# Kernel optimization log

Hardware: AMD Instinct MI355X
Metric: run time of the kernel (lower is better)

Reference implementation:

```python
import jax, jax.numpy as jnp
import numpy as np
from jax import lax
from jax.scipy.special import logsumexp

B, S, H, T, V = 64, 512, 768, 16, 30522


def setup_inputs() -> dict:
    key = jax.random.key(0)
    ks = jax.random.split(key, 8)
    src = jax.random.randint(ks[0], (B, S), 0, V, dtype=jnp.int32)
    label = jax.random.randint(ks[1], (B, S), 0, T, dtype=jnp.int32)
    padding_mask = jnp.ones((B, S), jnp.int32)
    emb_table = jax.random.normal(ks[2], (V, H), jnp.float32) * 0.02
    W = jax.random.normal(ks[3], (H, T), jnp.float32) * 0.02
    b = jnp.zeros((T,), jnp.float32)
    start_trans = jax.random.normal(ks[4], (T,), jnp.float32) * 0.1
    end_trans = jax.random.normal(ks[5], (T,), jnp.float32) * 0.1
    transitions = jax.random.normal(ks[6], (T, T), jnp.float32) * 0.1
    return dict(src=src, label=label, padding_mask=padding_mask,
                emb_table=emb_table, W=W, b=b, start_trans=start_trans,
                end_trans=end_trans, transitions=transitions)


def crf_log_likelihood(emissions, tags, mask, start_trans, end_trans, transitions):
    # emissions [S,B,T], tags [S,B] int, mask [S,B] float. torchcrf reduction='sum'.
    nS, nB, nT = emissions.shape
    barange = jnp.arange(nB)
    # --- numerator: score of the gold path ---
    score0 = start_trans[tags[0]] + emissions[0, barange, tags[0]]
    def num_step(score, xs):
        em_t, tag_prev, tag_t, m = xs
        s = transitions[tag_prev, tag_t] + em_t[barange, tag_t]
        return score + s * m, None
    num, _ = lax.scan(num_step, score0, (emissions[1:], tags[:-1], tags[1:], mask[1:]))
    seq_len = jnp.sum(mask, axis=0).astype(jnp.int32)          # [B]
    last_tags = tags[seq_len - 1, barange]
    num = num + end_trans[last_tags]
    # --- denominator: forward algorithm (per-step logsumexp) ---
    alpha0 = start_trans[None, :] + emissions[0]               # [B,T]
    def den_step(alpha, xs):
        em_t, m = xs
        nxt = logsumexp(alpha[:, :, None] + transitions[None, :, :] + em_t[:, None, :], axis=1)
        return jnp.where(m[:, None] > 0, nxt, alpha), None
    alpha, _ = lax.scan(den_step, alpha0, (emissions[1:], mask[1:]))
    den = logsumexp(alpha + end_trans[None, :], axis=1)
    return jnp.sum(num - den)


def viterbi_decode(emissions, start_trans, end_trans, transitions):
    # emissions [S,B,T]; full-length decode (no mask, as in the original call).
    score0 = start_trans[None, :] + emissions[0]               # [B,T]
    def fwd_step(score, em_t):
        br = score[:, :, None] + transitions[None, :, :] + em_t[:, None, :]  # [B,T,T]
        return jnp.max(br, axis=1), jnp.argmax(br, axis=1)
    score, hist = lax.scan(fwd_step, score0, emissions[1:])    # hist [S-1,B,T]
    last = jnp.argmax(score + end_trans[None, :], axis=1)      # [B]
    def back_step(tag, h_t):
        prev = jnp.take_along_axis(h_t, tag[:, None], axis=1)[:, 0]
        return prev, prev
    _, prevs = lax.scan(back_step, last, hist, reverse=True)   # prevs[t] = tag at t
    return jnp.concatenate([prevs, last[None, :]], axis=0)     # [S,B]


def reference(src, label, padding_mask, emb_table, W, b, start_trans, end_trans, transitions):
    bs = src.shape[0]
    emb = emb_table[src]                                       # [B,S,H]
    logits = jnp.einsum('bsh,ht->bst', emb, W) + b             # [B,S,T] (dropout in eval = identity)
    emissions = jnp.transpose(logits, (1, 0, 2))               # [S,B,T]
    tags = label.T                                             # [S,B]
    mask = padding_mask.T.astype(logits.dtype)                 # [S,B]
    ll = crf_log_likelihood(emissions, tags, mask, start_trans, end_trans, transitions)
    loss = -ll / bs
    predict = viterbi_decode(emissions, start_trans, end_trans, transitions).T  # [B,S]
    label_flat = label.reshape(-1)
    pred_flat = predict.reshape(-1).astype(label_flat.dtype)
    label_mask = (label_flat > 0).astype(label_flat.dtype)
    pred_flat = pred_flat * label_mask
    correct = jnp.sum((pred_flat == label_flat).astype(jnp.float32))
    return loss, correct, pred_flat, label_flat
```

## Files before the change

kernel.cpp:

```cpp
#include <hip/hip_runtime.h>

#define Bq 64
#define Sq 512
#define Hq 768
#define Tq 16
#define Vq 30522
#define EMP 516
#define WLP 20

typedef unsigned int u32;
typedef unsigned long long u64;

__device__ __forceinline__ float bperm_f(float v, int byteidx) {
    return __int_as_float(__builtin_amdgcn_ds_bpermute(byteidx, __float_as_int(v)));
}
template <int CTRL>
__device__ __forceinline__ int dpp_i(int v) {
    return __builtin_amdgcn_mov_dpp(v, CTRL, 0xF, 0xF, true);
}
template <int CTRL>
__device__ __forceinline__ u32 dpp_u(u32 v) { return (u32)dpp_i<CTRL>((int)v); }
template <int CTRL>
__device__ __forceinline__ float dpp_f(float v) {
    return __int_as_float(dpp_i<CTRL>(__float_as_int(v)));
}

#define QX1 0xB1
#define QX2 0x4E
#define RR4  0x124
#define RR8  0x128
#define RR12 0x12C

#if defined(__gfx950__) && __has_builtin(__builtin_amdgcn_permlane32_swap) && __has_builtin(__builtin_amdgcn_permlane16_swap)
#define HAVE_PL 1
#else
#define HAVE_PL 0
#endif

#if HAVE_PL
__device__ __forceinline__ u32 xlane32(u32 x) {
    auto r = __builtin_amdgcn_permlane32_swap((int)x, (int)x, false, false);
    return ((u32)r[0]) ^ ((u32)r[1]) ^ x;
}
__device__ __forceinline__ u32 xlane16(u32 x) {
    auto r = __builtin_amdgcn_permlane16_swap((int)x, (int)x, false, false);
    return ((u32)r[0]) ^ ((u32)r[1]) ^ x;
}
__device__ __forceinline__ void gather4(u32 x, bool swA, bool swB,
                                        u32& q0, u32& q1, u32& q2, u32& q3) {
    u32 t  = xlane32(x);
    u32 y  = dpp_u<QX2>(t);
    u32 z  = swA ? y : x;
    u32 t2 = xlane16(z);
    u32 y2 = dpp_u<QX1>(t2);
    q0 = swB ? y2 : z;
    q1 = dpp_u<RR4>(q0);
    q2 = dpp_u<RR8>(q0);
    q3 = dpp_u<RR12>(q0);
}
#endif

__device__ __forceinline__ u32 packnib(u32 d) {
    u32 y = d | (d >> 4);
    y &= 0x00FF00FFu;
    y = (y | (y >> 8)) & 0xFFFFu;
    return y;
}
__device__ __forceinline__ u32 nib64(u64 f, u32 s) {
    return ((u32)(f >> (s << 2))) & 15u;
}

__global__ __launch_bounds__(256, 2) void k_table(const float* __restrict__ emb,
                                                  const float* __restrict__ W,
                                                  const float* __restrict__ bias,
                                                  float* __restrict__ table,
                                                  float* __restrict__ out) {
    if (blockIdx.x == 0 && threadIdx.x == 0) out[1] = 0.0f;
    __shared__ float WL[Hq * WLP];
    const int tid = threadIdx.x;

    #pragma unroll
    for (int k = 0; k < 12; ++k) {
        int idx = tid + (k << 8);
        float4 v = *reinterpret_cast<const float4*>(W + idx * 4);
        *reinterpret_cast<float4*>(&WL[(idx >> 2) * WLP + ((idx & 3) << 2)]) = v;
    }
    __syncthreads();

    const int r_loc = tid >> 2;
    const int q     = tid & 3;
    const int v     = blockIdx.x * 64 + r_loc;
    const int vc    = v < Vq ? v : Vq - 1;
    const float* arow = emb + (size_t)vc * Hq;

    float acc[16];
    #pragma unroll
    for (int t = 0; t < 16; ++t) acc[t] = 0.0f;

    float4 buf[8];
    #pragma unroll
    for (int u = 0; u < 8; ++u)
        buf[u] = *reinterpret_cast<const float4*>(arow + (q + 4 * u) * 4);

    for (int k6 = 0; k6 < 6; ++k6) {
        #pragma unroll
        for (int u = 0; u < 8; ++u) {
            const int k = k6 * 8 + u;
            float4 av = buf[u];
            if (k + 8 < 48)
                buf[u] = *reinterpret_cast<const float4*>(arow + (q + 4 * (k + 8)) * 4);
            const int hb = (q + 4 * k) * 4;
            #pragma unroll
            for (int a = 0; a < 4; ++a) {
                float s = (a == 0) ? av.x : (a == 1) ? av.y : (a == 2) ? av.z : av.w;
                const float* wr = &WL[(hb + a) * WLP];
                float4 w0 = *reinterpret_cast<const float4*>(wr);
                float4 w1 = *reinterpret_cast<const float4*>(wr + 4);
                float4 w2 = *reinterpret_cast<const float4*>(wr + 8);
                float4 w3 = *reinterpret_cast<const float4*>(wr + 12);
                acc[0]  = fmaf(s, w0.x, acc[0]);
                acc[1]  = fmaf(s, w0.y, acc[1]);
                acc[2]  = fmaf(s, w0.z, acc[2]);
                acc[3]  = fmaf(s, w0.w, acc[3]);
                acc[4]  = fmaf(s, w1.x, acc[4]);
                acc[5]  = fmaf(s, w1.y, acc[5]);
                acc[6]  = fmaf(s, w1.z, acc[6]);
                acc[7]  = fmaf(s, w1.w, acc[7]);
                acc[8]  = fmaf(s, w2.x, acc[8]);
                acc[9]  = fmaf(s, w2.y, acc[9]);
                acc[10] = fmaf(s, w2.z, acc[10]);
                acc[11] = fmaf(s, w2.w, acc[11]);
                acc[12] = fmaf(s, w3.x, acc[12]);
                acc[13] = fmaf(s, w3.y, acc[13]);
                acc[14] = fmaf(s, w3.z, acc[14]);
                acc[15] = fmaf(s, w3.w, acc[15]);
            }
        }
    }
    #pragma unroll
    for (int t = 0; t < 16; ++t) {
        acc[t] += dpp_f<QX1>(acc[t]);
        acc[t] += dpp_f<QX2>(acc[t]);
    }
    if (v < Vq) {
        float4 bv = *reinterpret_cast<const float4*>(bias + q * 4);
        float4 o = make_float4(acc[q * 4] + bv.x, acc[q * 4 + 1] + bv.y,
                               acc[q * 4 + 2] + bv.z, acc[q * 4 + 3] + bv.w);
        *reinterpret_cast<float4*>(table + (size_t)v * Tq + q * 4) = o;
    }
}

__global__ __launch_bounds__(64) void k_scan(const int* __restrict__ src,
                                             const int* __restrict__ label,
                                             const int* __restrict__ pmask,
                                             const float* __restrict__ table,
                                             const float* __restrict__ start_t,
                                             const float* __restrict__ end_t,
                                             const float* __restrict__ trans,
                                             float* __restrict__ nd,
                                             float* __restrict__ out) {
    __shared__ __align__(16) float emT[Tq * EMP];
    __shared__ __align__(16) unsigned char hist8[Sq * Tq];
    __shared__ int srcl[Sq];
    __shared__ int labl[Sq];
    __shared__ __align__(8) unsigned char predi8[Sq];

    const int lane = threadIdx.x;
    const int b = blockIdx.x & 63;
    const bool vit = blockIdx.x >= 64;

    #pragma unroll
    for (int k = 0; k < 8; ++k) {
        int t = lane + (k << 6);
        srcl[t] = src[b * Sq + t];
        labl[t] = label[b * Sq + t];
    }
    __syncthreads();
    if (!vit) {
        #pragma unroll 4
        for (int k = 0; k < 128; ++k) {
            int idx = lane + (k << 6);
            int t = idx >> 4, jj = idx & 15;
            emT[jj * EMP + t] = __expf(table[(size_t)srcl[t] * Tq + jj]) * 0.0625f;
        }
    } else {
        #pragma unroll 4
        for (int k = 0; k < 128; ++k) {
            int idx = lane + (k << 6);
            int t = idx >> 4, jj = idx & 15;
            emT[jj * EMP + t] = table[(size_t)srcl[t] * Tq + jj];
        }
    }
    __syncthreads();

    const int j = lane >> 2;
    const int g = lane & 3;
    const float4* emrow = reinterpret_cast<const float4*>(&emT[j * EMP]);

    const bool swA = (((lane >> 5) ^ (lane >> 1)) & 1) != 0;
    const bool swB = (((lane >> 4) ^ lane) & 1) != 0;
    int k0 = 0, k1 = 1, k2 = 2, k3 = 3;
    bool fastok = false;
#if HAVE_PL
    {
        u32 q0, q1, q2, q3;
        gather4((u32)j, swA, swB, q0, q1, q2, q3);
        bool ok = ((q0 >> 2) == (u32)g) && ((q1 >> 2) == (u32)g) &&
                  ((q2 >> 2) == (u32)g) && ((q3 >> 2) == (u32)g);
        u32 cov = (1u << (q0 & 3)) | (1u << (q1 & 3)) | (1u << (q2 & 3)) | (1u << (q3 & 3));
        ok = ok && (cov == 15u);
        fastok = (__all(ok ? 1 : 0) != 0);
        if (fastok) { k0 = (int)(q0 & 3); k1 = (int)(q1 & 3); k2 = (int)(q2 & 3); k3 = (int)(q3 & 3); }
    }
#endif
    const int bidx0 = (g << 6), bidx1 = (g << 6) + 16, bidx2 = (g << 6) + 32, bidx3 = (g << 6) + 48;

    if (!vit) {
        float E0 = __expf(trans[(4 * g + k0) * Tq + j]);
        float E1 = __expf(trans[(4 * g + k1) * Tq + j]);
        float E2 = __expf(trans[(4 * g + k2) * Tq + j]);
        float E3 = __expf(trans[(4 * g + k3) * Tq + j]);

        float4 f0 = emrow[0];
        float p = __expf(start_t[j]) * f0.x * 16.0f;

#define DEN_STEP_PL(ff)  { u32 qa, qb, qc, qd;                                         \
            gather4(__float_as_uint(p), swA, swB, qa, qb, qc, qd);                     \
            float s = (__uint_as_float(qa) * E0 + __uint_as_float(qb) * E1)            \
                    + (__uint_as_float(qc) * E2 + __uint_as_float(qd) * E3);           \
            s += dpp_f<QX1>(s);  s += dpp_f<QX2>(s);  p = s * (ff); }
#define DEN_STEP_BP(ff)  { float p0 = bperm_f(p, bidx0), p1 = bperm_f(p, bidx1),       \
                                 p2 = bperm_f(p, bidx2), p3 = bperm_f(p, bidx3);       \
            float s = (p0 * E0 + p1 * E1) + (p2 * E2 + p3 * E3);                       \
            s += dpp_f<QX1>(s);  s += dpp_f<QX2>(s);  p = s * (ff); }

#if HAVE_PL
        if (fastok) {
            DEN_STEP_PL(f0.y) DEN_STEP_PL(f0.z) DEN_STEP_PL(f0.w)
            float4 fc = emrow[1];
            for (int t0 = 4; t0 < Sq; t0 += 4) {
                float4 fn;
                if (t0 + 4 < Sq) fn = emrow[(t0 >> 2) + 1];
                DEN_STEP_PL(fc.x) DEN_STEP_PL(fc.y) DEN_STEP_PL(fc.z) DEN_STEP_PL(fc.w)
                fc = fn;
            }
        } else
#endif
        {
            DEN_STEP_BP(f0.y) DEN_STEP_BP(f0.z) DEN_STEP_BP(f0.w)
            float4 fc = emrow[1];
            for (int t0 = 4; t0 < Sq; t0 += 4) {
                float4 fn;
                if (t0 + 4 < Sq) fn = emrow[(t0 >> 2) + 1];
                DEN_STEP_BP(fc.x) DEN_STEP_BP(fc.y) DEN_STEP_BP(fc.z) DEN_STEP_BP(fc.w)
                fc = fn;
            }
        }
        float val = p * __expf(end_t[j]);
        #pragma unroll
        for (int off = 1; off < 64; off <<= 1) val += __shfl_xor(val, off);
        float den = (float)(511.0 * 2.7725887222397811) + __logf(val * 0.25f);

        float numv = 0.0f;
        int sl = 0;
        #pragma unroll
        for (int k = 0; k < 8; ++k) {
            int t = lane + (k << 6);
            int tag = labl[t];
            int m = pmask[b * Sq + t];
            sl += m;
            float emtt = table[(size_t)srcl[t] * Tq + tag];
            if (t == 0) {
                numv += start_t[tag] + emtt;
            } else {
                int tp = labl[t - 1];
                numv += (float)m * (trans[tp * Tq + tag] + emtt);
            }
        }
        #pragma unroll
        for (int off = 1; off < 64; off <<= 1) {
            numv += __shfl_xor(numv, off);
            sl += __shfl_xor(sl, off);
        }
        if (lane == 0) {
            int last = labl[sl - 1];
            nd[b] = (numv + end_t[last]) - den;
        }
    } else {
        float T0 = trans[(4 * g + k0) * Tq + j];
        float T1 = trans[(4 * g + k1) * Tq + j];
        float T2 = trans[(4 * g + k2) * Tq + j];
        float T3 = trans[(4 * g + k3) * Tq + j];
        const int i0 = 4 * g + k0, i1 = 4 * g + k1, i2 = 4 * g + k2, i3 = 4 * g + k3;

#define VIT_STEP_PL(emv, th) { u32 qa, qb, qc, qd;                                     \
            gather4(__float_as_uint(sc), swA, swB, qa, qb, qc, qd);                    \
            float v0 = __uint_as_float(qa) + T0, v1 = __uint_as_float(qb) + T1;        \
            float v2 = __uint_as_float(qc) + T2, v3 = __uint_as_float(qd) + T3;        \
            float ml = fmaxf(fmaxf(v0, v1), fmaxf(v2, v3));                            \
            float m1 = fmaxf(ml, dpp_f<QX1>(ml));                                      \
            float mv = fmaxf(m1, dpp_f<QX2>(m1));                                      \
            sc = mv + (emv);                                                           \
            int c0 = (v0 == mv) ? i0 : 99, c1 = (v1 == mv) ? i1 : 99;                  \
            int c2 = (v2 == mv) ? i2 : 99, c3 = (v3 == mv) ? i3 : 99;                  \
            int li = min(min(c0, c1), min(c2, c3));                                    \
            li = min(li, dpp_i<QX1>(li));  li = min(li, dpp_i<QX2>(li));               \
            if (g == 0) hist8[(th) * Tq + j] = (unsigned char)li; }
#define VIT_STEP_BP(emv, th) { float v0 = bperm_f(sc, bidx0) + T0,                     \
                 v1 = bperm_f(sc, bidx1) + T1, v2 = bperm_f(sc, bidx2) + T2,           \
                 v3 = bperm_f(sc, bidx3) + T3;                                         \
            float ml = fmaxf(fmaxf(v0, v1), fmaxf(v2, v3));                            \
            float m1 = fmaxf(ml, dpp_f<QX1>(ml));                                      \
            float mv = fmaxf(m1, dpp_f<QX2>(m1));                                      \
            sc = mv + (emv);                                                           \
            int c0 = (v0 == mv) ? i0 : 99, c1 = (v1 == mv) ? i1 : 99;                  \
            int c2 = (v2 == mv) ? i2 : 99, c3 = (v3 == mv) ? i3 : 99;                  \
            int li = min(min(c0, c1), min(c2, c3));                                    \
            li = min(li, dpp_i<QX1>(li));  li = min(li, dpp_i<QX2>(li));               \
            if (g == 0) hist8[(th) * Tq + j] = (unsigned char)li; }

        float4 e0 = emrow[0];
        float sc = start_t[j] + e0.x;
#if HAVE_PL
        if (fastok) {
            VIT_STEP_PL(e0.y, 0) VIT_STEP_PL(e0.z, 1) VIT_STEP_PL(e0.w, 2)
            float4 fc = emrow[1];
            for (int t0 = 4; t0 < Sq; t0 += 4) {
                float4 fn;
                if (t0 + 4 < Sq) fn = emrow[(t0 >> 2) + 1];
                VIT_STEP_PL(fc.x, t0 - 1) VIT_STEP_PL(fc.y, t0)
                VIT_STEP_PL(fc.z, t0 + 1) VIT_STEP_PL(fc.w, t0 + 2)
                fc = fn;
            }
        } else
#endif
        {
            VIT_STEP_BP(e0.y, 0) VIT_STEP_BP(e0.z, 1) VIT_STEP_BP(e0.w, 2)
            float4 fc = emrow[1];
            for (int t0 = 4; t0 < Sq; t0 += 4) {
                float4 fn;
                if (t0 + 4 < Sq) fn = emrow[(t0 >> 2) + 1];
                VIT_STEP_BP(fc.x, t0 - 1) VIT_STEP_BP(fc.y, t0)
                VIT_STEP_BP(fc.z, t0 + 1) VIT_STEP_BP(fc.w, t0 + 2)
                fc = fn;
            }
        }
        float fv = sc + end_t[j];
        int fi = j;
        #pragma unroll
        for (int off = 4; off < 64; off <<= 1) {
            float ov = __shfl_xor(fv, off);
            int oi = __shfl_xor(fi, off);
            bool take = (ov > fv) || (ov == fv && oi < fi);
            fv = take ? ov : fv;
            fi = take ? oi : fi;
        }
        if (lane < 16) hist8[511 * Tq + lane] = (unsigned char)lane;
        __syncthreads();

        u64 rp[8];
        #pragma unroll
        for (int k = 0; k < 8; ++k) {
            uint4 rw = *reinterpret_cast<const uint4*>(&hist8[(lane * 8 + k) * Tq]);
            u32 lo = packnib(rw.x) | (packnib(rw.y) << 16);
            u32 hi = packnib(rw.z) | (packnib(rw.w) << 16);
            rp[k] = (u64)lo | ((u64)hi << 32);
        }
        u64 F = rp[7];
        #pragma unroll
        for (int k = 6; k >= 0; --k) {
            u64 nf = 0;
            #pragma unroll
            for (int e = 0; e < 16; ++e) {
                u32 s = (u32)(F >> (e * 4)) & 15u;
                nf |= ((u64)nib64(rp[k], s)) << (e * 4);
            }
            F = nf;
        }
        u32 Flo = (u32)F, Fhi = (u32)(F >> 32);

        u32 pk[8] = {0, 0, 0, 0, 0, 0, 0, 0};
        u32 E = (u32)fi;
        #pragma unroll 64
        for (int c = 63; c >= 0; --c) {
            u64 Fc = ((u64)(u32)__builtin_amdgcn_readlane((int)Fhi, c) << 32)
                   | (u64)(u32)__builtin_amdgcn_readlane((int)Flo, c);
            pk[c >> 3] |= E << ((c & 7) * 4);
            E = nib64(Fc, E);
        }

        u32 a0 = (lane & 8) ? pk[1] : pk[0];
        u32 a1 = (lane & 8) ? pk[3] : pk[2];
        u32 a2 = (lane & 8) ? pk[5] : pk[4];
        u32 a3 = (lane & 8) ? pk[7] : pk[6];
        u32 b0 = (lane & 16) ? a1 : a0;
        u32 b1 = (lane & 16) ? a3 : a2;
        u32 c0s = (lane & 32) ? b1 : b0;
        u32 cur = (c0s >> ((lane & 7) * 4)) & 15u;
        u32 w0 = 0, w1 = 0;
        #pragma unroll
        for (int k = 7; k >= 0; --k) {
            cur = nib64(rp[k], cur);
            if (k >= 4) w1 |= cur << ((k - 4) * 8);
            else        w0 |= cur << (k * 8);
        }
        *reinterpret_cast<uint2*>(&predi8[lane * 8]) = make_uint2(w0, w1);
        __syncthreads();

        int cnt = 0;
        #pragma unroll
        for (int k = 0; k < 8; ++k) {
            int s_ = lane + (k << 6);
            int lab = labl[s_];
            int pr = (int)predi8[s_];
            int mpr = lab > 0 ? pr : 0;
            out[2 + b * Sq + s_] = (float)mpr;
            out[2 + Bq * Sq + b * Sq + s_] = (float)lab;
            cnt += (mpr == lab) ? 1 : 0;
        }
        #pragma unroll
        for (int off = 1; off < 64; off <<= 1) cnt += __shfl_xor(cnt, off);
        if (lane == 0) atomicAdd(out + 1, (float)cnt);
    }
}

__global__ __launch_bounds__(64) void k_final(const float* __restrict__ nd,
                                              float* __restrict__ out) {
    float v = nd[threadIdx.x];
    #pragma unroll
    for (int off = 1; off < 64; off <<= 1) v += __shfl_xor(v, off);
    if (threadIdx.x == 0) out[0] = -v * (1.0f / (float)Bq);
}

extern "C" void kernel_launch(void* const* d_in, const int* in_sizes, int n_in,
                              void* d_out, int out_size, void* d_ws, size_t ws_size,
                              hipStream_t stream) {
    const int*   src   = (const int*)d_in[0];
    const int*   label = (const int*)d_in[1];
    const int*   pmask = (const int*)d_in[2];
    const float* emb   = (const float*)d_in[3];
    const float* W     = (const float*)d_in[4];
    const float* bias  = (const float*)d_in[5];
    const float* st    = (const float*)d_in[6];
    const float* en    = (const float*)d_in[7];
    const float* tr    = (const float*)d_in[8];
    float* out = (float*)d_out;

    float* table = (float*)d_ws;
    float* nd    = table + (size_t)Vq * Tq;

    const int nblk = (Vq + 63) / 64;
    k_table<<<nblk, 256, 0, stream>>>(emb, W, bias, table, out);
    k_scan<<<128, 64, 0, stream>>>(src, label, pmask, table, st, en, tr, nd, out);
    k_final<<<1, 64, 0, stream>>>(nd, out);
}
```

Baseline: 109.2 us.

## Pack four sequences per wave with a 16-lane DPP all-gather scan

Reworks the CRF forward and Viterbi scans so each 64-lane wave processes four batch rows. Each row uses 16 lanes, one per tag, and gathers all 16 previous-step scores with quad and row-rotate DPP moves, replacing the 4-lane-per-tag permlane-swap scheme. The up-front staging of emissions into LDS is removed. Emissions are now read from the global table inside the loop, prefetched eight steps ahead, and exponentiated per step. The scan kernel drops from 128 blocks to 32, trading fewer, heavier waves and more per-step instructions for a shorter cross-lane dependency chain and no staging phase.

```diff
diff --git a/kernel.cpp b/kernel.cpp
--- a/kernel.cpp
+++ b/kernel.cpp
@@ -5,7 +5,6 @@
 #define Hq 768
 #define Tq 16
 #define Vq 30522
-#define EMP 516
 #define WLP 20
 
 typedef unsigned int u32;
@@ -19,46 +18,16 @@
     return __builtin_amdgcn_mov_dpp(v, CTRL, 0xF, 0xF, true);
 }
 template <int CTRL>
-__device__ __forceinline__ u32 dpp_u(u32 v) { return (u32)dpp_i<CTRL>((int)v); }
-template <int CTRL>
 __device__ __forceinline__ float dpp_f(float v) {
     return __int_as_float(dpp_i<CTRL>(__float_as_int(v)));
 }
 
 #define QX1 0xB1
 #define QX2 0x4E
+#define QX3 0x1B
 #define RR4  0x124
 #define RR8  0x128
 #define RR12 0x12C
-
-#if defined(__gfx950__) && __has_builtin(__builtin_amdgcn_permlane32_swap) && __has_builtin(__builtin_amdgcn_permlane16_swap)
-#define HAVE_PL 1
-#else
-#define HAVE_PL 0
-#endif
-
-#if HAVE_PL
-__device__ __forceinline__ u32 xlane32(u32 x) {
-    auto r = __builtin_amdgcn_permlane32_swap((int)x, (int)x, false, false);
-    return ((u32)r[0]) ^ ((u32)r[1]) ^ x;
-}
-__device__ __forceinline__ u32 xlane16(u32 x) {
-    auto r = __builtin_amdgcn_permlane16_swap((int)x, (int)x, false, false);
-    return ((u32)r[0]) ^ ((u32)r[1]) ^ x;
-}
-__device__ __forceinline__ void gather4(u32 x, bool swA, bool swB,
-                                        u32& q0, u32& q1, u32& q2, u32& q3) {
-    u32 t  = xlane32(x);
-    u32 y  = dpp_u<QX2>(t);
-    u32 z  = swA ? y : x;
-    u32 t2 = xlane16(z);
-    u32 y2 = dpp_u<QX1>(t2);
-    q0 = swB ? y2 : z;
-    q1 = dpp_u<RR4>(q0);
-    q2 = dpp_u<RR8>(q0);
-    q3 = dpp_u<RR12>(q0);
-}
-#endif
 
 __device__ __forceinline__ u32 packnib(u32 d) {
     u32 y = d | (d >> 4);
@@ -150,6 +119,68 @@
     }
 }
 
+
+#define G16_DPP(PV) \
+      float r1 = dpp_f<QX1>(PV), r2 = dpp_f<QX2>(PV), r3 = dpp_f<QX3>(PV); \
+      float r4 = dpp_f<RR4>(PV), r8v = dpp_f<RR8>(PV), r12v = dpp_f<RR12>(PV); \
+      float r5 = dpp_f<QX1>(r4), r6 = dpp_f<QX2>(r4), r7 = dpp_f<QX3>(r4); \
+      float r9 = dpp_f<QX1>(r8v), r10 = dpp_f<QX2>(r8v), r11 = dpp_f<QX3>(r8v); \
+      float r13 = dpp_f<QX1>(r12v), r14 = dpp_f<QX2>(r12v), r15 = dpp_f<QX3>(r12v);
+
+#define G16_BP(PV) \
+      const int rb_ = (lane & 48) << 2; \
+      float r1 = bperm_f(PV, rb_ + (pm[1] << 2)),  r2 = bperm_f(PV, rb_ + (pm[2] << 2)); \
+      float r3 = bperm_f(PV, rb_ + (pm[3] << 2)),  r4 = bperm_f(PV, rb_ + (pm[4] << 2)); \
+      float r5 = bperm_f(PV, rb_ + (pm[5] << 2)),  r6 = bperm_f(PV, rb_ + (pm[6] << 2)); \
+      float r7 = bperm_f(PV, rb_ + (pm[7] << 2)),  r8v = bperm_f(PV, rb_ + (pm[8] << 2)); \
+      float r9 = bperm_f(PV, rb_ + (pm[9] << 2)),  r10 = bperm_f(PV, rb_ + (pm[10] << 2)); \
+      float r11 = bperm_f(PV, rb_ + (pm[11] << 2)), r12v = bperm_f(PV, rb_ + (pm[12] << 2)); \
+      float r13 = bperm_f(PV, rb_ + (pm[13] << 2)), r14 = bperm_f(PV, rb_ + (pm[14] << 2)); \
+      float r15 = bperm_f(PV, rb_ + (pm[15] << 2));
+
+#define DEN_BODY \
+      float ff = __expf(em) * 0.0625f; \
+      float a0 = P * Wt[0];    a0 = fmaf(r1, Wt[1], a0);   a0 = fmaf(r2, Wt[2], a0);   a0 = fmaf(r3, Wt[3], a0); \
+      float a1 = r4 * Wt[4];   a1 = fmaf(r5, Wt[5], a1);   a1 = fmaf(r6, Wt[6], a1);   a1 = fmaf(r7, Wt[7], a1); \
+      float a2 = r8v * Wt[8];  a2 = fmaf(r9, Wt[9], a2);   a2 = fmaf(r10, Wt[10], a2); a2 = fmaf(r11, Wt[11], a2); \
+      float a3 = r12v * Wt[12]; a3 = fmaf(r13, Wt[13], a3); a3 = fmaf(r14, Wt[14], a3); a3 = fmaf(r15, Wt[15], a3); \
+      P = ((a0 + a1) + (a2 + a3)) * ff;
+
+#define VIT_BODY \
+      float v0 = P + Wt[0],    v1 = r1 + Wt[1],   v2 = r2 + Wt[2],   v3 = r3 + Wt[3]; \
+      float v4 = r4 + Wt[4],   v5 = r5 + Wt[5],   v6 = r6 + Wt[6],   v7 = r7 + Wt[7]; \
+      float v8 = r8v + Wt[8],  v9 = r9 + Wt[9],   v10 = r10 + Wt[10], v11 = r11 + Wt[11]; \
+      float v12 = r12v + Wt[12], v13 = r13 + Wt[13], v14 = r14 + Wt[14], v15 = r15 + Wt[15]; \
+      float mv = fmaxf(fmaxf(fmaxf(fmaxf(v0, v1), fmaxf(v2, v3)), fmaxf(fmaxf(v4, v5), fmaxf(v6, v7))), \
+                       fmaxf(fmaxf(fmaxf(v8, v9), fmaxf(v10, v11)), fmaxf(fmaxf(v12, v13), fmaxf(v14, v15)))); \
+      int c0 = (v0 == mv) ? st[0] : 99,  c1 = (v1 == mv) ? st[1] : 99; \
+      int c2 = (v2 == mv) ? st[2] : 99,  c3 = (v3 == mv) ? st[3] : 99; \
+      int c4 = (v4 == mv) ? st[4] : 99,  c5 = (v5 == mv) ? st[5] : 99; \
+      int c6 = (v6 == mv) ? st[6] : 99,  c7 = (v7 == mv) ? st[7] : 99; \
+      int c8 = (v8 == mv) ? st[8] : 99,  c9 = (v9 == mv) ? st[9] : 99; \
+      int c10 = (v10 == mv) ? st[10] : 99, c11 = (v11 == mv) ? st[11] : 99; \
+      int c12 = (v12 == mv) ? st[12] : 99, c13 = (v13 == mv) ? st[13] : 99; \
+      int c14 = (v14 == mv) ? st[14] : 99, c15 = (v15 == mv) ? st[15] : 99; \
+      int li = min(min(min(min(c0, c1), min(c2, c3)), min(min(c4, c5), min(c6, c7))), \
+                   min(min(min(c8, c9), min(c10, c11)), min(min(c12, c13), min(c14, c15)))); \
+      P = mv + em; \
+      hbase[(t - 1) * Tq] = (unsigned char)li;
+
+#define SCAN_LOOP(GATHER, BODY) \
+  for (int bi = 0; bi < 64; ++bi) { \
+    _Pragma("unroll") \
+    for (int u = 0; u < 8; ++u) { \
+      const int t = 1 + bi * 8 + u; \
+      if (t <= 511) { \
+        float em = raw[u]; \
+        { int tp = t + 8; if (tp > 511) tp = 511; \
+          raw[u] = table[(size_t)srcl[(b4 << 9) + tp] * Tq + j]; } \
+        GATHER(P); \
+        BODY; \
+      } \
+    } \
+  }
+
 __global__ __launch_bounds__(64) void k_scan(const int* __restrict__ src,
                                              const int* __restrict__ label,
                                              const int* __restrict__ pmask,
@@ -159,264 +190,195 @@
                                              const float* __restrict__ trans,
                                              float* __restrict__ nd,
                                              float* __restrict__ out) {
-    __shared__ __align__(16) float emT[Tq * EMP];
-    __shared__ __align__(16) unsigned char hist8[Sq * Tq];
-    __shared__ int srcl[Sq];
-    __shared__ int labl[Sq];
-    __shared__ __align__(8) unsigned char predi8[Sq];
+    __shared__ int srcl[4 * Sq];
+    __shared__ int labl[4 * Sq];
+    __shared__ __align__(16) unsigned char hist8[4 * Sq * Tq];
+    __shared__ __align__(8) unsigned char predi8[4 * Sq];
 
     const int lane = threadIdx.x;
-    const int b = blockIdx.x & 63;
-    const bool vit = blockIdx.x >= 64;
-
-    #pragma unroll
-    for (int k = 0; k < 8; ++k) {
-        int t = lane + (k << 6);
-        srcl[t] = src[b * Sq + t];
-        labl[t] = label[b * Sq + t];
+    const int b4 = lane >> 4;
+    const int j  = lane & 15;
+    const bool vit = blockIdx.x >= 16;
+    const int bb = (vit ? blockIdx.x - 16 : blockIdx.x) * 4;
+    const int batch = bb + b4;
+
+    #pragma unroll
+    for (int k = 0; k < 32; ++k) {
+        int idx = lane + (k << 6);
+        int bb4 = idx >> 9, t = idx & 511;
+        srcl[idx] = src[(bb + bb4) * Sq + t];
+        labl[idx] = label[(bb + bb4) * Sq + t];
     }
     __syncthreads();
+
+    int pm[16];
+    bool fast;
+    {
+        float x = __int_as_float(j);
+        G16_DPP(x);
+        pm[0] = j;
+        pm[1] = __float_as_int(r1);  pm[2] = __float_as_int(r2);  pm[3] = __float_as_int(r3);
+        pm[4] = __float_as_int(r4);  pm[5] = __float_as_int(r5);  pm[6] = __float_as_int(r6);
+        pm[7] = __float_as_int(r7);  pm[8] = __float_as_int(r8v); pm[9] = __float_as_int(r9);
+        pm[10] = __float_as_int(r10); pm[11] = __float_as_int(r11); pm[12] = __float_as_int(r12v);
+        pm[13] = __float_as_int(r13); pm[14] = __float_as_int(r14); pm[15] = __float_as_int(r15);
+        u32 cov = 0;
+        bool inr = true;
+        #pragma unroll
+        for (int s = 0; s < 16; ++s) {
+            inr = inr && (pm[s] >= 0) && (pm[s] < 16);
+            cov |= 1u << (pm[s] & 15);
+        }
+        fast = (__all((inr && cov == 0xFFFFu) ? 1 : 0) != 0);
+        if (!fast) {
+            pm[0] = j;
+            #pragma unroll
+            for (int s = 1; s < 16; ++s) pm[s] = (j + s) & 15;
+        }
+    }
+
+    float Wt[16];
+    int st[16];
+    #pragma unroll
+    for (int s = 0; s < 16; ++s) {
+        float tv = trans[pm[s] * Tq + j];
+        Wt[s] = vit ? tv : __expf(tv);
+        st[s] = pm[s];
+    }
+
+    float em00 = table[(size_t)srcl[b4 << 9] * Tq + j];
+    float P = vit ? (start_t[j] + em00) : __expf(start_t[j] + em00);
+
+    float raw[8];
+    #pragma unroll
+    for (int u = 0; u < 8; ++u) {
+        int t = 1 + u; if (t > 511) t = 511;
+        raw[u] = table[(size_t)srcl[(b4 << 9) + t] * Tq + j];
+    }
+
+    unsigned char* hbase = hist8 + b4 * (Sq * Tq) + j;
+
     if (!vit) {
-        #pragma unroll 4
-        for (int k = 0; k < 128; ++k) {
-            int idx = lane + (k << 6);
-            int t = idx >> 4, jj = idx & 15;
-            emT[jj * EMP + t] = __expf(table[(size_t)srcl[t] * Tq + jj]) * 0.0625f;
-        }
-    } else {
-        #pragma unroll 4
-        for (int k = 0; k < 128; ++k) {
-            int idx = lane + (k << 6);
-            int t = idx >> 4, jj = idx & 15;
-            emT[jj * EMP + t] = table[(size_t)srcl[t] * Tq + jj];
-        }
-    }
-    __syncthreads();
-
-    const int j = lane >> 2;
-    const int g = lane & 3;
-    const float4* emrow = reinterpret_cast<const float4*>(&emT[j * EMP]);
-
-    const bool swA = (((lane >> 5) ^ (lane >> 1)) & 1) != 0;
-    const bool swB = (((lane >> 4) ^ lane) & 1) != 0;
-    int k0 = 0, k1 = 1, k2 = 2, k3 = 3;
-    bool fastok = false;
-#if HAVE_PL
-    {
-        u32 q0, q1, q2, q3;
-        gather4((u32)j, swA, swB, q0, q1, q2, q3);
-        bool ok = ((q0 >> 2) == (u32)g) && ((q1 >> 2) == (u32)g) &&
-                  ((q2 >> 2) == (u32)g) && ((q3 >> 2) == (u32)g);
-        u32 cov = (1u << (q0 & 3)) | (1u << (q1 & 3)) | (1u << (q2 & 3)) | (1u << (q3 & 3));
-        ok = ok && (cov == 15u);
-        fastok = (__all(ok ? 1 : 0) != 0);
-        if (fastok) { k0 = (int)(q0 & 3); k1 = (int)(q1 & 3); k2 = (int)(q2 & 3); k3 = (int)(q3 & 3); }
-    }
-#endif
-    const int bidx0 = (g << 6), bidx1 = (g << 6) + 16, bidx2 = (g << 6) + 32, bidx3 = (g << 6) + 48;
-
-    if (!vit) {
-        float E0 = __expf(trans[(4 * g + k0) * Tq + j]);
-        float E1 = __expf(trans[(4 * g + k1) * Tq + j]);
-        float E2 = __expf(trans[(4 * g + k2) * Tq + j]);
-        float E3 = __expf(trans[(4 * g + k3) * Tq + j]);
-
-        float4 f0 = emrow[0];
-        float p = __expf(start_t[j]) * f0.x * 16.0f;
-
-#define DEN_STEP_PL(ff)  { u32 qa, qb, qc, qd;                                         \
-            gather4(__float_as_uint(p), swA, swB, qa, qb, qc, qd);                     \
-            float s = (__uint_as_float(qa) * E0 + __uint_as_float(qb) * E1)            \
-                    + (__uint_as_float(qc) * E2 + __uint_as_float(qd) * E3);           \
-            s += dpp_f<QX1>(s);  s += dpp_f<QX2>(s);  p = s * (ff); }
-#define DEN_STEP_BP(ff)  { float p0 = bperm_f(p, bidx0), p1 = bperm_f(p, bidx1),       \
-                                 p2 = bperm_f(p, bidx2), p3 = bperm_f(p, bidx3);       \
-            float s = (p0 * E0 + p1 * E1) + (p2 * E2 + p3 * E3);                       \
-            s += dpp_f<QX1>(s);  s += dpp_f<QX2>(s);  p = s * (ff); }
-
-#if HAVE_PL
-        if (fastok) {
-            DEN_STEP_PL(f0.y) DEN_STEP_PL(f0.z) DEN_STEP_PL(f0.w)
-            float4 fc = emrow[1];
-            for (int t0 = 4; t0 < Sq; t0 += 4) {
-                float4 fn;
-                if (t0 + 4 < Sq) fn = emrow[(t0 >> 2) + 1];
-                DEN_STEP_PL(fc.x) DEN_STEP_PL(fc.y) DEN_STEP_PL(fc.z) DEN_STEP_PL(fc.w)
-                fc = fn;
-            }
-        } else
-#endif
-        {
-            DEN_STEP_BP(f0.y) DEN_STEP_BP(f0.z) DEN_STEP_BP(f0.w)
-            float4 fc = emrow[1];
-            for (int t0 = 4; t0 < Sq; t0 += 4) {
-                float4 fn;
-                if (t0 + 4 < Sq) fn = emrow[(t0 >> 2) + 1];
-                DEN_STEP_BP(fc.x) DEN_STEP_BP(fc.y) DEN_STEP_BP(fc.z) DEN_STEP_BP(fc.w)
-                fc = fn;
-            }
-        }
-        float val = p * __expf(end_t[j]);
-        #pragma unroll
-        for (int off = 1; off < 64; off <<= 1) val += __shfl_xor(val, off);
-        float den = (float)(511.0 * 2.7725887222397811) + __logf(val * 0.25f);
+        if (fast) { SCAN_LOOP(G16_DPP, DEN_BODY) }
+        else      { SCAN_LOOP(G16_BP, DEN_BODY) }
+
+        float val = P * __expf(end_t[j]);
+        val += dpp_f<QX1>(val); val += dpp_f<QX2>(val);
+        val += dpp_f<RR4>(val); val += dpp_f<RR8>(val);
+        float den = (float)(511.0 * 2.7725887222397811) + __logf(val);
 
         float numv = 0.0f;
         int sl = 0;
         #pragma unroll
-        for (int k = 0; k < 8; ++k) {
-            int t = lane + (k << 6);
-            int tag = labl[t];
-            int m = pmask[b * Sq + t];
+        for (int k = 0; k < 32; ++k) {
+            int t = j + (k << 4);
+            int tag = labl[(b4 << 9) + t];
+            int m = pmask[batch * Sq + t];
             sl += m;
-            float emtt = table[(size_t)srcl[t] * Tq + tag];
+            float emtt = table[(size_t)srcl[(b4 << 9) + t] * Tq + tag];
             if (t == 0) {
                 numv += start_t[tag] + emtt;
             } else {
-                int tp = labl[t - 1];
+                int tp = labl[(b4 << 9) + t - 1];
                 numv += (float)m * (trans[tp * Tq + tag] + emtt);
             }
         }
-        #pragma unroll
-        for (int off = 1; off < 64; off <<= 1) {
-            numv += __shfl_xor(numv, off);
-            sl += __shfl_xor(sl, off);
-        }
-        if (lane == 0) {
-            int last = labl[sl - 1];
-            nd[b] = (numv + end_t[last]) - den;
+        numv += dpp_f<QX1>(numv); numv += dpp_f<QX2>(numv);
+        numv += dpp_f<RR4>(numv); numv += dpp_f<RR8>(numv);
+        sl += dpp_i<QX1>(sl); sl += dpp_i<QX2>(sl);
+        sl += dpp_i<RR4>(sl); sl += dpp_i<RR8>(sl);
+        if (j == 0) {
+            int last = labl[(b4 << 9) + sl - 1];
+            nd[batch] = (numv + end_t[last]) - den;
         }
     } else {
-        float T0 = trans[(4 * g + k0) * Tq + j];
-        float T1 = trans[(4 * g + k1) * Tq + j];
-        float T2 = trans[(4 * g + k2) * Tq + j];
-        float T3 = trans[(4 * g + k3) * Tq + j];
-        const int i0 = 4 * g + k0, i1 = 4 * g + k1, i2 = 4 * g + k2, i3 = 4 * g + k3;
-
-#define VIT_STEP_PL(emv, th) { u32 qa, qb, qc, qd;                                     \
-            gather4(__float_as_uint(sc), swA, swB, qa, qb, qc, qd);                    \
-            float v0 = __uint_as_float(qa) + T0, v1 = __uint_as_float(qb) + T1;        \
-            float v2 = __uint_as_float(qc) + T2, v3 = __uint_as_float(qd) + T3;        \
-            float ml = fmaxf(fmaxf(v0, v1), fmaxf(v2, v3));                            \
-            float m1 = fmaxf(ml, dpp_f<QX1>(ml));                                      \
-            float mv = fmaxf(m1, dpp_f<QX2>(m1));                                      \
-            sc = mv + (emv);                                                           \
-            int c0 = (v0 == mv) ? i0 : 99, c1 = (v1 == mv) ? i1 : 99;                  \
-            int c2 = (v2 == mv) ? i2 : 99, c3 = (v3 == mv) ? i3 : 99;                  \
-            int li = min(min(c0, c1), min(c2, c3));                                    \
-            li = min(li, dpp_i<QX1>(li));  li = min(li, dpp_i<QX2>(li));               \
-            if (g == 0) hist8[(th) * Tq + j] = (unsigned char)li; }
-#define VIT_STEP_BP(emv, th) { float v0 = bperm_f(sc, bidx0) + T0,                     \
-                 v1 = bperm_f(sc, bidx1) + T1, v2 = bperm_f(sc, bidx2) + T2,           \
-                 v3 = bperm_f(sc, bidx3) + T3;                                         \
-            float ml = fmaxf(fmaxf(v0, v1), fmaxf(v2, v3));                            \
-            float m1 = fmaxf(ml, dpp_f<QX1>(ml));                                      \
-            float mv = fmaxf(m1, dpp_f<QX2>(m1));                                      \
-            sc = mv + (emv);                                                           \
-            int c0 = (v0 == mv) ? i0 : 99, c1 = (v1 == mv) ? i1 : 99;                  \
-            int c2 = (v2 == mv) ? i2 : 99, c3 = (v3 == mv) ? i3 : 99;                  \
-            int li = min(min(c0, c1), min(c2, c3));                                    \
-            li = min(li, dpp_i<QX1>(li));  li = min(li, dpp_i<QX2>(li));               \
-            if (g == 0) hist8[(th) * Tq + j] = (unsigned char)li; }
-
-        float4 e0 = emrow[0];
-        float sc = start_t[j] + e0.x;
-#if HAVE_PL
-        if (fastok) {
-            VIT_STEP_PL(e0.y, 0) VIT_STEP_PL(e0.z, 1) VIT_STEP_PL(e0.w, 2)
-            float4 fc = emrow[1];
-            for (int t0 = 4; t0 < Sq; t0 += 4) {
-                float4 fn;
-                if (t0 + 4 < Sq) fn = emrow[(t0 >> 2) + 1];
-                VIT_STEP_PL(fc.x, t0 - 1) VIT_STEP_PL(fc.y, t0)
-                VIT_STEP_PL(fc.z, t0 + 1) VIT_STEP_PL(fc.w, t0 + 2)
-                fc = fn;
-            }
-        } else
-#endif
-        {
-            VIT_STEP_BP(e0.y, 0) VIT_STEP_BP(e0.z, 1) VIT_STEP_BP(e0.w, 2)
-            float4 fc = emrow[1];
-            for (int t0 = 4; t0 < Sq; t0 += 4) {
-                float4 fn;
-                if (t0 + 4 < Sq) fn = emrow[(t0 >> 2) + 1];
-                VIT_STEP_BP(fc.x, t0 - 1) VIT_STEP_BP(fc.y, t0)
-                VIT_STEP_BP(fc.z, t0 + 1) VIT_STEP_BP(fc.w, t0 + 2)
-                fc = fn;
-            }
-        }
-        float fv = sc + end_t[j];
+        if (fast) { SCAN_LOOP(G16_DPP, VIT_BODY) }
+        else      { SCAN_LOOP(G16_BP, VIT_BODY) }
+
+        float fv = P + end_t[j];
         int fi = j;
         #pragma unroll
-        for (int off = 4; off < 64; off <<= 1) {
+        for (int off = 1; off < 16; off <<= 1) {
             float ov = __shfl_xor(fv, off);
             int oi = __shfl_xor(fi, off);
             bool take = (ov > fv) || (ov == fv && oi < fi);
             fv = take ? ov : fv;
             fi = take ? oi : fi;
         }
-        if (lane < 16) hist8[511 * Tq + lane] = (unsigned char)lane;
+        if (lane < 16) {
+            hist8[(0 << 13) + 511 * 16 + lane] = (unsigned char)lane;
+            hist8[(1 << 13) + 511 * 16 + lane] = (unsigned char)lane;
+            hist8[(2 << 13) + 511 * 16 + lane] = (unsigned char)lane;
+            hist8[(3 << 13) + 511 * 16 + lane] = (unsigned char)lane;
+        }
         __syncthreads();
 
-        u64 rp[8];
-        #pragma unroll
-        for (int k = 0; k < 8; ++k) {
-            uint4 rw = *reinterpret_cast<const uint4*>(&hist8[(lane * 8 + k) * Tq]);
-            u32 lo = packnib(rw.x) | (packnib(rw.y) << 16);
-            u32 hi = packnib(rw.z) | (packnib(rw.w) << 16);
-            rp[k] = (u64)lo | ((u64)hi << 32);
-        }
-        u64 F = rp[7];
-        #pragma unroll
-        for (int k = 6; k >= 0; --k) {
-            u64 nf = 0;
-            #pragma unroll
-            for (int e = 0; e < 16; ++e) {
-                u32 s = (u32)(F >> (e * 4)) & 15u;
-                nf |= ((u64)nib64(rp[k], s)) << (e * 4);
-            }
-            F = nf;
-        }
-        u32 Flo = (u32)F, Fhi = (u32)(F >> 32);
-
-        u32 pk[8] = {0, 0, 0, 0, 0, 0, 0, 0};
-        u32 E = (u32)fi;
-        #pragma unroll 64
-        for (int c = 63; c >= 0; --c) {
-            u64 Fc = ((u64)(u32)__builtin_amdgcn_readlane((int)Fhi, c) << 32)
-                   | (u64)(u32)__builtin_amdgcn_readlane((int)Flo, c);
-            pk[c >> 3] |= E << ((c & 7) * 4);
-            E = nib64(Fc, E);
-        }
-
-        u32 a0 = (lane & 8) ? pk[1] : pk[0];
-        u32 a1 = (lane & 8) ? pk[3] : pk[2];
-        u32 a2 = (lane & 8) ? pk[5] : pk[4];
-        u32 a3 = (lane & 8) ? pk[7] : pk[6];
-        u32 b0 = (lane & 16) ? a1 : a0;
-        u32 b1 = (lane & 16) ? a3 : a2;
-        u32 c0s = (lane & 32) ? b1 : b0;
-        u32 cur = (c0s >> ((lane & 7) * 4)) & 15u;
-        u32 w0 = 0, w1 = 0;
-        #pragma unroll
-        for (int k = 7; k >= 0; --k) {
-            cur = nib64(rp[k], cur);
-            if (k >= 4) w1 |= cur << ((k - 4) * 8);
-            else        w0 |= cur << (k * 8);
-        }
-        *reinterpret_cast<uint2*>(&predi8[lane * 8]) = make_uint2(w0, w1);
+        #pragma unroll
+        for (int b4i = 0; b4i < 4; ++b4i) {
+            const unsigned char* hb = hist8 + (b4i << 13);
+            u64 rp[8];
+            #pragma unroll
+            for (int k = 0; k < 8; ++k) {
+                uint4 rw = *reinterpret_cast<const uint4*>(hb + ((lane * 8 + k) << 4));
+                u32 lo = packnib(rw.x) | (packnib(rw.y) << 16);
+                u32 hi = packnib(rw.z) | (packnib(rw.w) << 16);
+                rp[k] = (u64)lo | ((u64)hi << 32);
+            }
+            u64 F = rp[7];
+            #pragma unroll
+            for (int k = 6; k >= 0; --k) {
+                u64 nf = 0;
+                #pragma unroll
+                for (int e = 0; e < 16; ++e) {
+                    u32 s = (u32)(F >> (e * 4)) & 15u;
+                    nf |= ((u64)nib64(rp[k], s)) << (e * 4);
+                }
+                F = nf;
+            }
+            u32 Flo = (u32)F, Fhi = (u32)(F >> 32);
+
+            u32 pk[8] = {0, 0, 0, 0, 0, 0, 0, 0};
+            u32 E = (u32)__builtin_amdgcn_readlane(fi, b4i * 16);
+            #pragma unroll 64
+            for (int c = 63; c >= 0; --c) {
+                u64 Fc = ((u64)(u32)__builtin_amdgcn_readlane((int)Fhi, c) << 32)
+                       | (u64)(u32)__builtin_amdgcn_readlane((int)Flo, c);
+                pk[c >> 3] |= E << ((c & 7) * 4);
+                E = nib64(Fc, E);
+            }
+
+            u32 a0 = (lane & 8) ? pk[1] : pk[0];
+            u32 a1 = (lane & 8) ? pk[3] : pk[2];
+            u32 a2 = (lane & 8) ? pk[5] : pk[4];
+            u32 a3 = (lane & 8) ? pk[7] : pk[6];
+            u32 b0 = (lane & 16) ? a1 : a0;
+            u32 b1 = (lane & 16) ? a3 : a2;
+            u32 c0s = (lane & 32) ? b1 : b0;
+            u32 cur = (c0s >> ((lane & 7) * 4)) & 15u;
+            u32 w0 = 0, w1 = 0;
+            #pragma unroll
+            for (int k = 7; k >= 0; --k) {
+                cur = nib64(rp[k], cur);
+                if (k >= 4) w1 |= cur << ((k - 4) * 8);
+                else        w0 |= cur << (k * 8);
+            }
+            *reinterpret_cast<uint2*>(&predi8[(b4i << 9) + lane * 8]) = make_uint2(w0, w1);
+        }
         __syncthreads();
 
         int cnt = 0;
         #pragma unroll
-        for (int k = 0; k < 8; ++k) {
-            int s_ = lane + (k << 6);
-            int lab = labl[s_];
-            int pr = (int)predi8[s_];
-            int mpr = lab > 0 ? pr : 0;
-            out[2 + b * Sq + s_] = (float)mpr;
-            out[2 + Bq * Sq + b * Sq + s_] = (float)lab;
-            cnt += (mpr == lab) ? 1 : 0;
+        for (int b4i = 0; b4i < 4; ++b4i) {
+            #pragma unroll
+            for (int k = 0; k < 8; ++k) {
+                int s_ = lane + (k << 6);
+                int lab = labl[(b4i << 9) + s_];
+                int pr = (int)predi8[(b4i << 9) + s_];
+                int mpr = lab > 0 ? pr : 0;
+                out[2 + (bb + b4i) * Sq + s_] = (float)mpr;
+                out[2 + Bq * Sq + (bb + b4i) * Sq + s_] = (float)lab;
+                cnt += (mpr == lab) ? 1 : 0;
+            }
         }
         #pragma unroll
         for (int off = 1; off < 64; off <<= 1) cnt += __shfl_xor(cnt, off);
@@ -451,6 +413,6 @@
 
     const int nblk = (Vq + 63) / 64;
     k_table<<<nblk, 256, 0, stream>>>(emb, W, bias, table, out);
-    k_scan<<<128, 64, 0, stream>>>(src, label, pmask, table, st, en, tr, nd, out);
+    k_scan<<<32, 64, 0, stream>>>(src, label, pmask, table, st, en, tr, nd, out);
     k_final<<<1, 64, 0, stream>>>(nd, out);
 }
```

After: 139.8 us. 28.0% more time.
